# Performance work log

Hardware: AMD Instinct MI355X
Metric: run time of the kernel (lower is better)

The kernel has to match this reference:

```python
import jax, jax.numpy as jnp
import numpy as np

TOP_K = 2  # k in TopKGate


def setup_inputs() -> dict:
    key = jax.random.key(0)
    k1, k2, k3 = jax.random.split(key, 3)
    B, S, H, E = 4, 2048, 1024, 8
    hidden_states = jax.random.normal(k1, (B, S, H), dtype=jnp.float32)
    Wg = jax.random.normal(k2, (H, E), dtype=jnp.float32) * (H ** -0.5)
    We = jax.random.normal(k3, (E, H, H), dtype=jnp.float32) * (H ** -0.5)
    be = jnp.zeros((E, H), dtype=jnp.float32)
    return {"hidden_states": hidden_states, "Wg": Wg, "We": We, "be": be}


def reference(hidden_states, Wg, We, be):
    # hidden_states: [B, S, H]; Wg: [H, E]; We: [E, H, H]; be: [E, H]
    B, S, H = hidden_states.shape
    T = B * S
    x = hidden_states.reshape(T, H)

    # TopKGate: linear gate -> softmax -> top-k -> renormalize combine weights
    probs = jax.nn.softmax(x @ Wg, axis=-1)              # [T, E]
    top_vals, top_idx = jax.lax.top_k(probs, TOP_K)     # [T, K]
    gates = top_vals / jnp.sum(top_vals, axis=-1, keepdims=True)

    # Experts: run each token through each expert Linear, then gather top-k
    expert_out = jnp.einsum('th,ehd->etd', x, We) + be[:, None, :]  # [E, T, H]
    tok = jnp.arange(T)[:, None]                         # [T, 1]
    sel = expert_out[top_idx, tok, :]                    # [T, K, H]

    # Weighted combine over top-k experts
    out = jnp.sum(gates[..., None] * sel, axis=1)        # [T, H]
    return out.reshape(B, S, H)
```

## Files before the change

kernel.cpp:

```cpp
#include <hip/hip_runtime.h>
#include <hip/hip_bf16.h>

#define H 1024
#define NEXP 8
#define T_TOK 8192
#define CAP 8192
#define TM 128
#define TN 128
#define BK 32
#define TPB 32

typedef __bf16 bf16x8 __attribute__((ext_vector_type(8)));
typedef __bf16 bf16x4 __attribute__((ext_vector_type(4)));
typedef float f32x4 __attribute__((ext_vector_type(4)));

__device__ __forceinline__ void async16(void* lds, const void* g) {
    __builtin_amdgcn_global_load_lds(
        (const __attribute__((address_space(1))) void*)g,
        (__attribute__((address_space(3))) void*)lds, 16, 0, 0);
}

__global__ __launch_bounds__(256) void moe_route(
    const float* __restrict__ x, const float* __restrict__ Wg,
    __bf16* __restrict__ Xb, int* __restrict__ cnt,
    int* __restrict__ ltok, float* __restrict__ lgate,
    int* __restrict__ tsel, float* __restrict__ tgate) {
    const int tid  = threadIdx.x;
    const int lane = tid & 63;
    const int wave = tid >> 6;
    const int base = blockIdx.x * TPB;

    __shared__ int   sE[TPB * 2];
    __shared__ float sG[TPB * 2];
    __shared__ int   lcnt[NEXP], lbase[NEXP], lslot[TPB * 2];

    for (int i = 0; i < TPB / 4; ++i) {
        const int tl = wave * (TPB / 4) + i;
        const int t  = base + tl;
        const float* xr  = x  + (size_t)t * H;
        __bf16*      xbr = Xb + (size_t)t * H;
        float a[NEXP];
#pragma unroll
        for (int e = 0; e < NEXP; ++e) a[e] = 0.f;
#pragma unroll
        for (int j = 0; j < H / 64; ++j) {
            const int h = j * 64 + lane;
            const float xv = xr[h];
            xbr[h] = (__bf16)xv;
            const float4 w0 = *(const float4*)(Wg + h * NEXP);
            const float4 w1 = *(const float4*)(Wg + h * NEXP + 4);
            a[0] += xv * w0.x; a[1] += xv * w0.y; a[2] += xv * w0.z; a[3] += xv * w0.w;
            a[4] += xv * w1.x; a[5] += xv * w1.y; a[6] += xv * w1.z; a[7] += xv * w1.w;
        }
#pragma unroll
        for (int e = 0; e < NEXP; ++e) {
#pragma unroll
            for (int off = 32; off > 0; off >>= 1)
                a[e] += __shfl_xor(a[e], off, 64);
        }
        int i0 = 0;
#pragma unroll
        for (int e = 1; e < NEXP; ++e) if (a[e] > a[i0]) i0 = e;
        int i1 = (i0 == 0) ? 1 : 0;
#pragma unroll
        for (int e = 0; e < NEXP; ++e) if (e != i0 && a[e] > a[i1]) i1 = e;
        const float ex = __expf(a[i1] - a[i0]);
        const float g0 = 1.f / (1.f + ex);
        const float g1 = ex / (1.f + ex);
        if (lane == 0) {
            sE[tl * 2] = i0; sE[tl * 2 + 1] = i1;
            sG[tl * 2] = g0; sG[tl * 2 + 1] = g1;
        }
    }
    if (tid < NEXP) lcnt[tid] = 0;
    __syncthreads();
    if (tid < TPB * 2) lslot[tid] = atomicAdd(&lcnt[sE[tid]], 1);
    __syncthreads();
    if (tid < NEXP) lbase[tid] = lcnt[tid] ? atomicAdd(&cnt[tid], lcnt[tid]) : 0;
    __syncthreads();
    if (tid < TPB * 2) {
        const int e = sE[tid];
        const int s = lbase[e] + lslot[tid];
        const int t = base + (tid >> 1);
        ltok[e * CAP + s]  = t;
        lgate[e * CAP + s] = sG[tid];
        tsel[t * 2 + (tid & 1)]  = e * CAP + s;
        tgate[t * 2 + (tid & 1)] = sG[tid];
    }
}

__global__ __launch_bounds__(256) void cast_transpose_we(
    const float* __restrict__ We, __bf16* __restrict__ WeT) {
    __shared__ float tile[32][33];
    const int e = blockIdx.z;
    const int d0 = blockIdx.x * 32;
    const int h0 = blockIdx.y * 32;
    const int tx = threadIdx.x & 31;
    const int ty = threadIdx.x >> 5;
    const float* src = We + ((size_t)e << 20);
    __bf16* dst = WeT + ((size_t)e << 20);
#pragma unroll
    for (int r = 0; r < 4; ++r)
        tile[ty + r * 8][tx] = src[(size_t)(h0 + ty + r * 8) * H + d0 + tx];
    __syncthreads();
#pragma unroll
    for (int r = 0; r < 4; ++r)
        dst[(size_t)(d0 + ty + r * 8) * H + h0 + tx] = (__bf16)tile[tx][ty + r * 8];
}

__global__ __launch_bounds__(256) void moe_gemm(
    const __bf16* __restrict__ Xb, const __bf16* __restrict__ WeT,
    const float* __restrict__ be, const int* __restrict__ cnt,
    const int* __restrict__ ltok, const float* __restrict__ lgate,
    __bf16* __restrict__ Eout) {
    const int e = blockIdx.z;
    const int ne = cnt[e];
    const int m0 = blockIdx.y * TM;
    if (m0 >= ne) return;
    const int n0 = blockIdx.x * TN;
    int off = 0;
    for (int i2 = 0; i2 < e; ++i2) off += cnt[i2];

    __shared__ __align__(16) __bf16 Al[TM * BK];
    __shared__ __align__(16) __bf16 Bl[TN * BK];
    __shared__ int tokL[TM];

    const int tid = threadIdx.x;
    const int lane = tid & 63;
    const int wave = tid >> 6;

    if (tid < TM) {
        const int gi = m0 + tid;
        tokL[tid] = (gi < ne) ? ltok[e * CAP + gi] : 0;
    }
    __syncthreads();

    const __bf16* Bt = WeT + ((size_t)e << 20);
    const int qr = lane >> 4;
    const int rr = lane & 15;
    const int wr = (wave >> 1) * 64;
    const int wc = (wave & 1) * 64;

    f32x4 acc[4][4];
    const f32x4 z = {0.f, 0.f, 0.f, 0.f};
#pragma unroll
    for (int i = 0; i < 4; ++i)
#pragma unroll
        for (int j = 0; j < 4; ++j) acc[i][j] = z;

    const int c0 = tid, c1 = tid + 256;
    const int ar0 = c0 >> 2, ak0 = (((c0 & 3) ^ ((c0 >> 3) & 3)) * 8);
    const int ar1 = c1 >> 2, ak1 = (((c1 & 3) ^ ((c1 >> 3) & 3)) * 8);
    const size_t arow0 = (size_t)tokL[ar0] * H;
    const size_t arow1 = (size_t)tokL[ar1] * H;
    const size_t brow0 = (size_t)(n0 + ar0) * H;
    const size_t brow1 = (size_t)(n0 + ar1) * H;

    for (int k0 = 0; k0 < H; k0 += BK) {
        async16(&Al[c0 * 8], Xb + arow0 + k0 + ak0);
        async16(&Al[c1 * 8], Xb + arow1 + k0 + ak1);
        async16(&Bl[c0 * 8], Bt + brow0 + k0 + ak0);
        async16(&Bl[c1 * 8], Bt + brow1 + k0 + ak1);
        __syncthreads();
        bf16x8 af[4], bfr[4];
#pragma unroll
        for (int i = 0; i < 4; ++i) {
            const int ra = wr + i * 16 + rr;
            af[i] = *(const bf16x8*)&Al[ra * BK + ((qr ^ ((ra >> 1) & 3)) * 8)];
        }
#pragma unroll
        for (int j = 0; j < 4; ++j) {
            const int rb = wc + j * 16 + rr;
            bfr[j] = *(const bf16x8*)&Bl[rb * BK + ((qr ^ ((rb >> 1) & 3)) * 8)];
        }
#pragma unroll
        for (int i = 0; i < 4; ++i)
#pragma unroll
            for (int j = 0; j < 4; ++j)
                acc[i][j] = __builtin_amdgcn_mfma_f32_16x16x32_bf16(af[i], bfr[j], acc[i][j], 0, 0, 0);
        __syncthreads();
    }

    float bev[4];
#pragma unroll
    for (int j = 0; j < 4; ++j) bev[j] = be[e * H + n0 + wc + j * 16 + rr];

#pragma unroll
    for (int i = 0; i < 4; ++i) {
#pragma unroll
        for (int reg = 0; reg < 4; ++reg) {
            const int rloc = wr + i * 16 + qr * 4 + reg;
            if (m0 + rloc < ne) {
                __bf16* orow = Eout + (size_t)(off + m0 + rloc) * H;
#pragma unroll
                for (int j = 0; j < 4; ++j) {
                    const int d = n0 + wc + j * 16 + rr;
                    orow[d] = (__bf16)(acc[i][j][reg] + bev[j]);
                }
            }
        }
    }
}

__global__ __launch_bounds__(256) void moe_combine(
    const __bf16* __restrict__ Eout, const int* __restrict__ cnt,
    const int* __restrict__ tsel, const float* __restrict__ tgate,
    float* __restrict__ out) {
    const int t = blockIdx.x;
    __shared__ int offs[NEXP];
    if (threadIdx.x < NEXP) {
        int o = 0;
        for (int i = 0; i < threadIdx.x; ++i) o += cnt[i];
        offs[threadIdx.x] = o;
    }
    __syncthreads();
    const int sel0 = tsel[t * 2],     sel1 = tsel[t * 2 + 1];
    const float g0 = tgate[t * 2],    g1   = tgate[t * 2 + 1];
    const int e0 = sel0 >> 13, s0 = sel0 & (CAP - 1);
    const int e1 = sel1 >> 13, s1 = sel1 & (CAP - 1);
    const __bf16* r0 = Eout + (size_t)(offs[e0] + s0) * H;
    const __bf16* r1 = Eout + (size_t)(offs[e1] + s1) * H;
    const int d = threadIdx.x * 4;
    const bf16x4 a = *(const bf16x4*)(r0 + d);
    const bf16x4 b = *(const bf16x4*)(r1 + d);
    float4 o;
    o.x = g0 * (float)a[0] + g1 * (float)b[0];
    o.y = g0 * (float)a[1] + g1 * (float)b[1];
    o.z = g0 * (float)a[2] + g1 * (float)b[2];
    o.w = g0 * (float)a[3] + g1 * (float)b[3];
    *(float4*)(out + (size_t)t * H + d) = o;
}

extern "C" void kernel_launch(void* const* d_in, const int* in_sizes, int n_in,
                              void* d_out, int out_size, void* d_ws, size_t ws_size,
                              hipStream_t stream) {
    const float* x  = (const float*)d_in[0];
    const float* Wg = (const float*)d_in[1];
    const float* We = (const float*)d_in[2];
    const float* be = (const float*)d_in[3];
    float* out = (float*)d_out;

    char* ws = (char*)d_ws;
    __bf16* Xb   = (__bf16*)ws;
    __bf16* WeT  = (__bf16*)(ws + ((size_t)16 << 20));
    __bf16* Eout = (__bf16*)(ws + ((size_t)32 << 20));
    char*   meta = ws + ((size_t)64 << 20);
    int*    cnt  = (int*)meta;
    int*    ltok = (int*)(meta + 256);
    float*  lgat = (float*)(meta + 256 + (size_t)NEXP * CAP * 4);
    int*    tsel = (int*)(meta + 256 + (size_t)NEXP * CAP * 8);
    float*  tgat = (float*)(meta + 256 + (size_t)NEXP * CAP * 8 + (size_t)T_TOK * 8);

    hipMemsetAsync(cnt, 0, NEXP * sizeof(int), stream);

    cast_transpose_we<<<dim3(H / 32, H / 32, NEXP), 256, 0, stream>>>(We, WeT);
    moe_route<<<T_TOK / TPB, 256, 0, stream>>>(x, Wg, Xb, cnt, ltok, lgat, tsel, tgat);
    moe_gemm<<<dim3(H / TN, T_TOK / TM, NEXP), 256, 0, stream>>>(Xb, WeT, be, cnt, ltok, lgat, Eout);
    moe_combine<<<T_TOK, 256, 0, stream>>>(Eout, cnt, tsel, tgat, out);
}
```

Measured before the change: 205.9 us.

## Vectorize route, transpose and combine kernels; pad expert counters

The routing kernel now loads x as float4 and writes bf16x4, and processes 16 tokens per block instead of 32 for more blocks. The We cast-transpose uses 64x64 tiles with float4 reads and bf16x4 writes. Combine handles one token per wave, four per block, with looping vector loads. Expert counters are padded to separate 128-byte lines to reduce atomic contention. These changes target memory-bound auxiliary kernels. The GEMM is untouched, so the overall effect depends on how much of the time those kernels account for.

```diff
diff --git a/kernel.cpp b/kernel.cpp
--- a/kernel.cpp
+++ b/kernel.cpp
@@ -8,7 +8,8 @@
 #define TM 128
 #define TN 128
 #define BK 32
-#define TPB 32
+#define TPB 16
+#define CNTSTRIDE 32
 
 typedef __bf16 bf16x8 __attribute__((ext_vector_type(8)));
 typedef __bf16 bf16x4 __attribute__((ext_vector_type(4)));
@@ -43,14 +44,21 @@
 #pragma unroll
         for (int e = 0; e < NEXP; ++e) a[e] = 0.f;
 #pragma unroll
-        for (int j = 0; j < H / 64; ++j) {
-            const int h = j * 64 + lane;
-            const float xv = xr[h];
-            xbr[h] = (__bf16)xv;
-            const float4 w0 = *(const float4*)(Wg + h * NEXP);
-            const float4 w1 = *(const float4*)(Wg + h * NEXP + 4);
-            a[0] += xv * w0.x; a[1] += xv * w0.y; a[2] += xv * w0.z; a[3] += xv * w0.w;
-            a[4] += xv * w1.x; a[5] += xv * w1.y; a[6] += xv * w1.z; a[7] += xv * w1.w;
+        for (int j = 0; j < H / 256; ++j) {
+            const int h = j * 256 + lane * 4;
+            const float4 xv = *(const float4*)(xr + h);
+            bf16x4 xo;
+            xo[0] = (__bf16)xv.x; xo[1] = (__bf16)xv.y;
+            xo[2] = (__bf16)xv.z; xo[3] = (__bf16)xv.w;
+            *(bf16x4*)(xbr + h) = xo;
+            const float xc[4] = {xv.x, xv.y, xv.z, xv.w};
+#pragma unroll
+            for (int c = 0; c < 4; ++c) {
+                const float4 w0 = *(const float4*)(Wg + (h + c) * NEXP);
+                const float4 w1 = *(const float4*)(Wg + (h + c) * NEXP + 4);
+                a[0] += xc[c] * w0.x; a[1] += xc[c] * w0.y; a[2] += xc[c] * w0.z; a[3] += xc[c] * w0.w;
+                a[4] += xc[c] * w1.x; a[5] += xc[c] * w1.y; a[6] += xc[c] * w1.z; a[7] += xc[c] * w1.w;
+            }
         }
 #pragma unroll
         for (int e = 0; e < NEXP; ++e) {
@@ -76,7 +84,7 @@
     __syncthreads();
     if (tid < TPB * 2) lslot[tid] = atomicAdd(&lcnt[sE[tid]], 1);
     __syncthreads();
-    if (tid < NEXP) lbase[tid] = lcnt[tid] ? atomicAdd(&cnt[tid], lcnt[tid]) : 0;
+    if (tid < NEXP) lbase[tid] = lcnt[tid] ? atomicAdd(&cnt[tid * CNTSTRIDE], lcnt[tid]) : 0;
     __syncthreads();
     if (tid < TPB * 2) {
         const int e = sE[tid];
@@ -91,21 +99,32 @@
 
 __global__ __launch_bounds__(256) void cast_transpose_we(
     const float* __restrict__ We, __bf16* __restrict__ WeT) {
-    __shared__ float tile[32][33];
-    const int e = blockIdx.z;
-    const int d0 = blockIdx.x * 32;
-    const int h0 = blockIdx.y * 32;
-    const int tx = threadIdx.x & 31;
-    const int ty = threadIdx.x >> 5;
+    __shared__ float t[64][65];
+    const int e  = blockIdx.z;
+    const int d0 = blockIdx.x * 64;
+    const int h0 = blockIdx.y * 64;
+    const int tx = threadIdx.x & 15;
+    const int ty = threadIdx.x >> 4;
     const float* src = We + ((size_t)e << 20);
     __bf16* dst = WeT + ((size_t)e << 20);
 #pragma unroll
-    for (int r = 0; r < 4; ++r)
-        tile[ty + r * 8][tx] = src[(size_t)(h0 + ty + r * 8) * H + d0 + tx];
-    __syncthreads();
-#pragma unroll
-    for (int r = 0; r < 4; ++r)
-        dst[(size_t)(d0 + ty + r * 8) * H + h0 + tx] = (__bf16)tile[tx][ty + r * 8];
+    for (int p = 0; p < 4; ++p) {
+        const int row = p * 16 + ty;
+        const float4 v = *(const float4*)(src + (size_t)(h0 + row) * H + d0 + tx * 4);
+        t[row][tx * 4 + 0] = v.x; t[row][tx * 4 + 1] = v.y;
+        t[row][tx * 4 + 2] = v.z; t[row][tx * 4 + 3] = v.w;
+    }
+    __syncthreads();
+#pragma unroll
+    for (int p = 0; p < 4; ++p) {
+        const int drow = p * 16 + ty;
+        bf16x4 o;
+        o[0] = (__bf16)t[tx * 4 + 0][drow];
+        o[1] = (__bf16)t[tx * 4 + 1][drow];
+        o[2] = (__bf16)t[tx * 4 + 2][drow];
+        o[3] = (__bf16)t[tx * 4 + 3][drow];
+        *(bf16x4*)(dst + (size_t)(d0 + drow) * H + h0 + tx * 4) = o;
+    }
 }
 
 __global__ __launch_bounds__(256) void moe_gemm(
@@ -114,12 +133,12 @@
     const int* __restrict__ ltok, const float* __restrict__ lgate,
     __bf16* __restrict__ Eout) {
     const int e = blockIdx.z;
-    const int ne = cnt[e];
+    const int ne = cnt[e * CNTSTRIDE];
     const int m0 = blockIdx.y * TM;
     if (m0 >= ne) return;
     const int n0 = blockIdx.x * TN;
     int off = 0;
-    for (int i2 = 0; i2 < e; ++i2) off += cnt[i2];
+    for (int i2 = 0; i2 < e; ++i2) off += cnt[i2 * CNTSTRIDE];
 
     __shared__ __align__(16) __bf16 Al[TM * BK];
     __shared__ __align__(16) __bf16 Bl[TN * BK];
@@ -206,29 +225,34 @@
     const __bf16* __restrict__ Eout, const int* __restrict__ cnt,
     const int* __restrict__ tsel, const float* __restrict__ tgate,
     float* __restrict__ out) {
-    const int t = blockIdx.x;
     __shared__ int offs[NEXP];
     if (threadIdx.x < NEXP) {
         int o = 0;
-        for (int i = 0; i < threadIdx.x; ++i) o += cnt[i];
+        for (int i = 0; i < (int)threadIdx.x; ++i) o += cnt[i * CNTSTRIDE];
         offs[threadIdx.x] = o;
     }
     __syncthreads();
-    const int sel0 = tsel[t * 2],     sel1 = tsel[t * 2 + 1];
-    const float g0 = tgate[t * 2],    g1   = tgate[t * 2 + 1];
+    const int wave = threadIdx.x >> 6, lane = threadIdx.x & 63;
+    const int t = blockIdx.x * 4 + wave;
+    const int sel0 = tsel[t * 2],  sel1 = tsel[t * 2 + 1];
+    const float g0 = tgate[t * 2], g1  = tgate[t * 2 + 1];
     const int e0 = sel0 >> 13, s0 = sel0 & (CAP - 1);
     const int e1 = sel1 >> 13, s1 = sel1 & (CAP - 1);
     const __bf16* r0 = Eout + (size_t)(offs[e0] + s0) * H;
     const __bf16* r1 = Eout + (size_t)(offs[e1] + s1) * H;
-    const int d = threadIdx.x * 4;
-    const bf16x4 a = *(const bf16x4*)(r0 + d);
-    const bf16x4 b = *(const bf16x4*)(r1 + d);
-    float4 o;
-    o.x = g0 * (float)a[0] + g1 * (float)b[0];
-    o.y = g0 * (float)a[1] + g1 * (float)b[1];
-    o.z = g0 * (float)a[2] + g1 * (float)b[2];
-    o.w = g0 * (float)a[3] + g1 * (float)b[3];
-    *(float4*)(out + (size_t)t * H + d) = o;
+    float* orow = out + (size_t)t * H;
+#pragma unroll
+    for (int c = 0; c < 4; ++c) {
+        const int d = c * 256 + lane * 4;
+        const bf16x4 a = *(const bf16x4*)(r0 + d);
+        const bf16x4 b = *(const bf16x4*)(r1 + d);
+        float4 o;
+        o.x = g0 * (float)a[0] + g1 * (float)b[0];
+        o.y = g0 * (float)a[1] + g1 * (float)b[1];
+        o.z = g0 * (float)a[2] + g1 * (float)b[2];
+        o.w = g0 * (float)a[3] + g1 * (float)b[3];
+        *(float4*)(orow + d) = o;
+    }
 }
 
 extern "C" void kernel_launch(void* const* d_in, const int* in_sizes, int n_in,
@@ -246,15 +270,15 @@
     __bf16* Eout = (__bf16*)(ws + ((size_t)32 << 20));
     char*   meta = ws + ((size_t)64 << 20);
     int*    cnt  = (int*)meta;
-    int*    ltok = (int*)(meta + 256);
-    float*  lgat = (float*)(meta + 256 + (size_t)NEXP * CAP * 4);
-    int*    tsel = (int*)(meta + 256 + (size_t)NEXP * CAP * 8);
-    float*  tgat = (float*)(meta + 256 + (size_t)NEXP * CAP * 8 + (size_t)T_TOK * 8);
-
-    hipMemsetAsync(cnt, 0, NEXP * sizeof(int), stream);
-
-    cast_transpose_we<<<dim3(H / 32, H / 32, NEXP), 256, 0, stream>>>(We, WeT);
+    int*    ltok = (int*)(meta + 1024);
+    float*  lgat = (float*)(meta + 1024 + (size_t)NEXP * CAP * 4);
+    int*    tsel = (int*)(meta + 1024 + (size_t)NEXP * CAP * 8);
+    float*  tgat = (float*)(meta + 1024 + (size_t)NEXP * CAP * 8 + (size_t)T_TOK * 8);
+
+    hipMemsetAsync(cnt, 0, NEXP * CNTSTRIDE * sizeof(int), stream);
+
+    cast_transpose_we<<<dim3(H / 64, H / 64, NEXP), 256, 0, stream>>>(We, WeT);
     moe_route<<<T_TOK / TPB, 256, 0, stream>>>(x, Wg, Xb, cnt, ltok, lgat, tsel, tgat);
     moe_gemm<<<dim3(H / TN, T_TOK / TM, NEXP), 256, 0, stream>>>(Xb, WeT, be, cnt, ltok, lgat, Eout);
-    moe_combine<<<T_TOK, 256, 0, stream>>>(Eout, cnt, tsel, tgat, out);
-}
+    moe_combine<<<T_TOK / 4, 256, 0, stream>>>(Eout, cnt, tsel, tgat, out);
+}
```

Measured after the change: 201.4 us. 2.2% less time.
